# Kernel optimization log

Hardware: AMD Instinct MI355X
Metric: run time of the kernel (lower is better)

Reference implementation:

```python
import jax, jax.numpy as jnp
import numpy as np

B, N, C, HEADS = 8, 1024, 768, 12
HW = 32  # H = W = 32, so H*W == N


def _layernorm(x, g, b, eps=1e-5):
    mu = x.mean(-1, keepdims=True)
    var = ((x - mu) ** 2).mean(-1, keepdims=True)
    return (x - mu) * jax.lax.rsqrt(var + eps) * g + b


def setup_inputs() -> dict:
    key = jax.random.key(0)
    ks = jax.random.split(key, 6)
    w = lambda k, shape: jax.random.normal(k, shape, dtype=jnp.float32) * 0.02
    return {
        "x": jax.random.normal(ks[0], (B, N, C), dtype=jnp.float32),
        "y": jax.random.normal(ks[1], (B, C, HW, HW), dtype=jnp.float32),
        "q_w": w(ks[2], (C, C)),
        "q_b": jnp.zeros((C,), jnp.float32),
        "kv_w": w(ks[3], (2 * C, C)),
        "kv_b": jnp.zeros((2 * C,), jnp.float32),
        "proj_w": w(ks[4], (C, C)),
        "proj_b": jnp.zeros((C,), jnp.float32),
        "ln_g": jnp.ones((C,), jnp.float32),
        "ln_b": jnp.zeros((C,), jnp.float32),
        "H": HW,
        "W": HW,
    }


def reference(x, y, q_w, q_b, kv_w, kv_b, proj_w, proj_b, ln_g, ln_b, H, W):
    Bn, Nn, Cn = x.shape
    hd = Cn // HEADS
    scale = hd ** -0.5  # qk_scale=None, c_ratio=1 -> head_dim**-0.5

    # gating tensors from y
    y1 = y.reshape(Bn, Cn, H * W).transpose(0, 2, 1)          # [B, N, C]
    y2 = _layernorm(y1, ln_g, ln_b)
    yq = jax.nn.sigmoid(y2 @ q_w.T + q_b)                      # [B, N, C]
    ykv = jax.nn.sigmoid(y2 @ kv_w.T + kv_b)                   # [B, N, 2C]

    # gated q: q2 = q0 + q0*yq
    q0 = x @ q_w.T + q_b
    q = (q0 + q0 * yq).reshape(Bn, Nn, HEADS, hd).transpose(0, 2, 1, 3)  # [B,h,N,d]

    # gated kv: kv2 = kv0*ykv + ykv
    kv0 = x @ kv_w.T + kv_b
    kv = (kv0 * ykv + ykv).reshape(Bn, Nn, 2, HEADS, hd).transpose(2, 0, 3, 1, 4)
    k, v = kv[0], kv[1]                                        # [B,h,N,d] each

    attn = jax.nn.softmax(jnp.einsum("bhqd,bhkd->bhqk", q, k) * scale, axis=-1)
    out = jnp.einsum("bhqk,bhkd->bhqd", attn, v)
    out = out.transpose(0, 2, 1, 3).reshape(Bn, Nn, Cn)
    return out @ proj_w.T + proj_b
```

## Files before the change

### kernel.cpp

```cpp
#include <hip/hip_runtime.h>
#include <stdint.h>

typedef __attribute__((ext_vector_type(4))) float f4;
typedef __attribute__((ext_vector_type(8))) short bf16x8;
typedef __attribute__((ext_vector_type(4))) unsigned short u16x4;
typedef unsigned short u16;

#define B_ 8
#define N_ 1024
#define C_ 768
#define NH 12
#define HD 64

__device__ __forceinline__ float bf2f(u16 v) {
  union { unsigned u; float f; } x; x.u = ((unsigned)v) << 16; return x.f;
}
__device__ __forceinline__ u16 f2bf(float f) {
  union { float f; unsigned u; } x; x.f = f;
  unsigned r = x.u + 0x7FFFu + ((x.u >> 16) & 1u);
  return (u16)(r >> 16);
}
__device__ __forceinline__ void g2l16(const u16* g, const u16* l) {
  __builtin_amdgcn_global_load_lds(
      (const __attribute__((address_space(1))) void*)(uintptr_t)g,
      (__attribute__((address_space(3))) void*)(uint32_t)(uintptr_t)l,
      16, 0, 0);
}

#define SW12() asm volatile("s_waitcnt vmcnt(12)" ::: "memory")
#define SW6()  asm volatile("s_waitcnt vmcnt(6)" ::: "memory")
#define SW4()  asm volatile("s_waitcnt vmcnt(4)" ::: "memory")
#define SW3()  asm volatile("s_waitcnt vmcnt(3)" ::: "memory")
#define SW0()  asm volatile("s_waitcnt vmcnt(0)" ::: "memory")
#define BARF()                              \
  do {                                      \
    __builtin_amdgcn_s_barrier();           \
    asm volatile("" ::: "memory");          \
    __builtin_amdgcn_sched_barrier(0);      \
  } while (0)

__global__ __launch_bounds__(256) void cvt_bf16(const float* __restrict__ s,
                                                u16* __restrict__ d, int n4) {
  int i = blockIdx.x * 256 + threadIdx.x;
  int stride = gridDim.x * 256;
  for (; i < n4; i += stride) {
    float4 v = ((const float4*)s)[i];
    u16x4 o;
    o.x = f2bf(v.x); o.y = f2bf(v.y); o.z = f2bf(v.z); o.w = f2bf(v.w);
    ((u16x4*)d)[i] = o;
  }
}

__global__ __launch_bounds__(256) void ln_stats(const float* __restrict__ y,
                                                float* __restrict__ mu,
                                                float* __restrict__ rs,
                                                int b0) {
  __shared__ float s1[4][64], s2[4][64];
  int t = threadIdx.x;
  int nl = t & 63, ch = t >> 6;
  int idx0 = b0 * N_ + blockIdx.x * 64;
  int b = idx0 >> 10, nb_ = idx0 & 1023;
  const float* p = y + (size_t)b * C_ * N_ + nb_ + nl;
  float s = 0.f, q = 0.f;
  int c0 = ch * 192;
  for (int c = c0; c < c0 + 192; ++c) {
    float v = p[(size_t)c * N_];
    s += v; q += v * v;
  }
  s1[ch][nl] = s; s2[ch][nl] = q;
  __syncthreads();
  if (t < 64) {
    float ts = s1[0][t] + s1[1][t] + s1[2][t] + s1[3][t];
    float tq = s2[0][t] + s2[1][t] + s2[2][t] + s2[3][t];
    float m = ts * (1.f / C_);
    float var = tq * (1.f / C_) - m * m;
    mu[idx0 + t] = m;
    rs[idx0 + t] = rsqrtf(fmaxf(var, 0.f) + 1e-5f);
  }
}

__global__ __launch_bounds__(256) void ln_apply(const float* __restrict__ y,
                                                const float* __restrict__ mu,
                                                const float* __restrict__ rs,
                                                const float* __restrict__ lg,
                                                const float* __restrict__ lb,
                                                u16* __restrict__ y2c,
                                                int b0) {
  __shared__ float tile[64][65];
  int t = threadIdx.x;
  int n0 = blockIdx.x * 64, c0 = blockIdx.y * 64;
  int bl = blockIdx.z, b = b0 + bl;
  int jc = (t & 15) * 4, ir = t >> 4;
  for (int r = 0; r < 4; ++r) {
    int i = ir + r * 16;
    float4 v = *(const float4*)(y + ((size_t)b * C_ + c0 + i) * N_ + n0 + jc);
    tile[i][jc] = v.x; tile[i][jc + 1] = v.y; tile[i][jc + 2] = v.z; tile[i][jc + 3] = v.w;
  }
  __syncthreads();
  for (int r = 0; r < 4; ++r) {
    int i = ir + r * 16;
    int n = n0 + i;
    float m = mu[b * N_ + n], rr = rs[b * N_ + n];
    float g0 = lg[c0 + jc],     b0f = lb[c0 + jc];
    float g1 = lg[c0 + jc + 1], b1f = lb[c0 + jc + 1];
    float g2 = lg[c0 + jc + 2], b2f = lb[c0 + jc + 2];
    float g3 = lg[c0 + jc + 3], b3f = lb[c0 + jc + 3];
    u16x4 o;
    o.x = f2bf((tile[jc][i] - m) * rr * g0 + b0f);
    o.y = f2bf((tile[jc + 1][i] - m) * rr * g1 + b1f);
    o.z = f2bf((tile[jc + 2][i] - m) * rr * g2 + b2f);
    o.w = f2bf((tile[jc + 3][i] - m) * rr * g3 + b3f);
    *(u16x4*)(y2c + ((size_t)bl * N_ + n) * C_ + c0 + jc) = o;
  }
}

__global__ __launch_bounds__(256, 2) void gemm_gate(
    const u16* __restrict__ xbc, const u16* __restrict__ y2c,
    const u16* __restrict__ qwb, const u16* __restrict__ kvwb,
    const float* __restrict__ qb_, const float* __restrict__ kvb_,
    u16* __restrict__ o_q, u16* __restrict__ o_k, u16* __restrict__ o_vT) {
  __shared__ u16 smem[36864];
  int t = threadIdx.x, l = t & 63;
  int quad = l >> 4, l15 = l & 15;
  int w = t >> 6, wm = w & 1, wn = w >> 1;
  int m0l = blockIdx.x * 128;
  int n0l = blockIdx.y * 128;

  const u16* wp; const float* bp; int sel, h0;
  if (n0l < C_) {
    wp = qwb + (size_t)n0l * C_; bp = qb_ + n0l; sel = 0; h0 = n0l >> 6;
  } else {
    int nk = n0l - C_;
    wp = kvwb + (size_t)nk * C_; bp = kvb_ + nk;
    sel = (nk < C_) ? 1 : 2;
    h0 = ((sel == 2) ? nk - C_ : nk) >> 6;
  }

  f4 accx[4][4], accy[4][4];
  for (int i = 0; i < 4; ++i)
    for (int j = 0; j < 4; ++j) {
      accx[i][j] = (f4){0.f, 0.f, 0.f, 0.f};
      accy[i][j] = (f4){0.f, 0.f, 0.f, 0.f};
    }

  int row = t >> 2;
  int colS = (((t & 3) ^ (row & 3)) * 8);
  const u16* gx = xbc + (size_t)(m0l + row) * C_ + colS;
  const u16* gy = y2c + (size_t)(m0l + row) * C_ + colS;
  const u16* gw = wp + (size_t)row * C_ + colS;
  int rsl = (quad ^ (l15 & 3)) * 8;

#define STAGE_G(OFF, kk)                                   \
  do {                                                     \
    u16* p_ = smem + (OFF);                                \
    g2l16(gx + (kk),           p_ + t * 8);                \
    g2l16(gx + (kk) + 64 * C_, p_ + 2048 + t * 8);         \
    g2l16(gy + (kk),           p_ + 4096 + t * 8);         \
    g2l16(gy + (kk) + 64 * C_, p_ + 6144 + t * 8);         \
    g2l16(gw + (kk),           p_ + 8192 + t * 8);         \
    g2l16(gw + (kk) + 64 * C_, p_ + 10240 + t * 8);        \
  } while (0)

#define COMPUTE_G(OFF)                                                        \
  do {                                                                        \
    const u16* base = smem + (OFF);                                           \
    bf16x8 afx[4], afy[4], bfr[4];                                            \
    for (int i = 0; i < 4; ++i) {                                             \
      int ra = (wm * 64 + i * 16 + l15) * 32 + rsl;                           \
      afx[i] = *(const bf16x8*)&base[ra];                                     \
      afy[i] = *(const bf16x8*)&base[4096 + ra];                              \
      int rb = (wn * 64 + i * 16 + l15) * 32 + rsl;                           \
      bfr[i] = *(const bf16x8*)&base[8192 + rb];                              \
    }                                                                         \
    for (int i = 0; i < 4; ++i)                                               \
      for (int j = 0; j < 4; ++j) {                                           \
        accx[i][j] = __builtin_amdgcn_mfma_f32_16x16x32_bf16(afx[i], bfr[j], accx[i][j], 0, 0, 0); \
        accy[i][j] = __builtin_amdgcn_mfma_f32_16x16x32_bf16(afy[i], bfr[j], accy[i][j], 0, 0, 0); \
      }                                                                       \
  } while (0)

#define STEP_G(i, OFF)                                        \
  do {                                                        \
    COMPUTE_G(OFF);                                           \
    BARF();                                                   \
    if ((i) < 21)      { STAGE_G(OFF, ((i) + 3) * 32); SW12(); } \
    else if ((i) == 21) SW6();                                \
    else if ((i) == 22) SW0();                                \
    BARF();                                                   \
  } while (0)

  STAGE_G(0, 0);
  STAGE_G(12288, 32);
  STAGE_G(24576, 64);
  SW12();
  BARF();
#pragma unroll
  for (int n = 0; n < 24; n += 3) {
    STEP_G(n, 0);
    STEP_G(n + 1, 12288);
    STEP_G(n + 2, 24576);
  }
#undef STEP_G
#undef STAGE_G
#undef COMPUTE_G

  const int PITCH = 136;
  for (int j = 0; j < 4; ++j) {
    int cloc = wn * 64 + j * 16 + l15;
    float bias = bp[cloc];
    for (int i = 0; i < 4; ++i) {
      int rb0 = wm * 64 + i * 16 + quad * 4;
      for (int r = 0; r < 4; ++r) {
        int rloc = rb0 + r;
        float vx = accx[i][j][r] + bias;
        float vy = accy[i][j][r] + bias;
        float gg = 1.f / (1.f + __expf(-vy));
        float val = (sel == 0) ? vx * (1.f + gg) : gg * (vx + 1.f);
        u16 bv = f2bf(val);
        if (sel == 2) smem[cloc * PITCH + rloc] = bv;
        else          smem[rloc * PITCH + cloc] = bv;
      }
    }
  }
  __syncthreads();
  {
    int rr = t >> 1, hh = t & 1;
    const u16* src = smem + rr * PITCH + hh * 64;
    u16* dst;
    if (sel == 2) {
      int h = h0 + (rr >> 6), d = rr & 63;
      int bl = m0l >> 10, nbase = m0l & 1023;
      dst = o_vT + (size_t)((bl * NH + h) * HD + d) * N_ + nbase + hh * 64;
    } else {
      int gml = m0l + rr;
      int bl = gml >> 10, n = gml & 1023;
      int h = h0 + hh;
      dst = (sel == 0 ? o_q : o_k) + (size_t)((bl * NH + h) * N_ + n) * HD;
    }
    for (int c = 0; c < 8; ++c) {
      bf16x8 v = *(const bf16x8*)(src + c * 8);
      *(bf16x8*)(dst + c * 8) = v;
    }
  }
}

__global__ __launch_bounds__(256) void attn(const u16* __restrict__ qoc,
                                            const u16* __restrict__ koc,
                                            const u16* __restrict__ vTc,
                                            u16* __restrict__ aoc) {
  __shared__ u16 Qs[4096], Ks[8192], Vs[8192];
  __shared__ u16 Ps[64 * 72];
  int t = threadIdx.x, l = t & 63, w = t >> 6;
  int quad = l >> 4, l15 = l & 15;
  int bhl = blockIdx.y;
  int bl = bhl / NH, h = bhl % NH;
  int q0 = blockIdx.x * 64;
  int sr = t >> 3;
  int swo = ((t & 7) ^ (sr & 7)) * 8;
  const u16* qbp = qoc + ((size_t)bhl * N_ + q0) * HD;
  const u16* kb = koc + (size_t)bhl * N_ * HD;
  const u16* vb = vTc + (size_t)bhl * HD * N_;

#define STAGE_KV(OFF, key0)                                                   \
  do {                                                                        \
    g2l16(kb + (size_t)((key0) + sr) * HD + swo,      Ks + (OFF) + t * 8);    \
    g2l16(kb + (size_t)((key0) + 32 + sr) * HD + swo, Ks + (OFF) + 2048 + t * 8); \
    g2l16(vb + (size_t)sr * N_ + (key0) + swo,        Vs + (OFF) + t * 8);    \
    g2l16(vb + (size_t)(32 + sr) * N_ + (key0) + swo, Vs + (OFF) + 2048 + t * 8); \
  } while (0)

  g2l16(qbp + sr * HD + swo,        Qs + t * 8);
  g2l16(qbp + (32 + sr) * HD + swo, Qs + 2048 + t * 8);
  STAGE_KV(0, 0);
  STAGE_KV(4096, 64);
  SW4();
  BARF();

  int sA = (quad ^ (l15 & 7)) * 8;
  int sB = sA ^ 32;
  bf16x8 aq0 = *(const bf16x8*)&Qs[(w * 16 + l15) * 64 + sA];
  bf16x8 aq1 = *(const bf16x8*)&Qs[(w * 16 + l15) * 64 + sB];
  f4 o[4];
  for (int i = 0; i < 4; ++i) o[i] = (f4){0.f, 0.f, 0.f, 0.f};
  f4 ls = (f4){0.f, 0.f, 0.f, 0.f};
  bf16x8 ones;
  for (int i = 0; i < 8; ++i) ones[i] = (short)0x3F80;

#define TILE_STEP(KOFF)                                                       \
  do {                                                                        \
    f4 s_[4];                                                                 \
    __builtin_amdgcn_s_setprio(1);                                            \
    for (int ni = 0; ni < 4; ++ni) {                                          \
      bf16x8 b0v = *(const bf16x8*)&Ks[(KOFF) + (ni * 16 + l15) * 64 + sA];   \
      bf16x8 b1v = *(const bf16x8*)&Ks[(KOFF) + (ni * 16 + l15) * 64 + sB];   \
      f4 z = (f4){0.f, 0.f, 0.f, 0.f};                                        \
      z = __builtin_amdgcn_mfma_f32_16x16x32_bf16(aq0, b0v, z, 0, 0, 0);      \
      z = __builtin_amdgcn_mfma_f32_16x16x32_bf16(aq1, b1v, z, 0, 0, 0);      \
      s_[ni] = z;                                                             \
    }                                                                         \
    __builtin_amdgcn_s_setprio(0);                                            \
    for (int ni = 0; ni < 4; ++ni)                                            \
      for (int r = 0; r < 4; ++r)                                             \
        Ps[(w * 16 + quad * 4 + r) * 72 + ni * 16 + l15] =                    \
            f2bf(__expf(s_[ni][r] * 0.125f));                                 \
    bf16x8 ap0 = *(const bf16x8*)&Ps[(w * 16 + l15) * 72 + quad * 8];         \
    bf16x8 ap1 = *(const bf16x8*)&Ps[(w * 16 + l15) * 72 + 32 + quad * 8];    \
    __builtin_amdgcn_s_setprio(1);                                            \
    for (int ni = 0; ni < 4; ++ni) {                                          \
      bf16x8 b0v = *(const bf16x8*)&Vs[(KOFF) + (ni * 16 + l15) * 64 + sA];   \
      bf16x8 b1v = *(const bf16x8*)&Vs[(KOFF) + (ni * 16 + l15) * 64 + sB];   \
      o[ni] = __builtin_amdgcn_mfma_f32_16x16x32_bf16(ap0, b0v, o[ni], 0, 0, 0); \
      o[ni] = __builtin_amdgcn_mfma_f32_16x16x32_bf16(ap1, b1v, o[ni], 0, 0, 0); \
    }                                                                         \
    ls = __builtin_amdgcn_mfma_f32_16x16x32_bf16(ap0, ones, ls, 0, 0, 0);     \
    ls = __builtin_amdgcn_mfma_f32_16x16x32_bf16(ap1, ones, ls, 0, 0, 0);     \
    __builtin_amdgcn_s_setprio(0);                                            \
  } while (0)

#pragma unroll
  for (int kt = 0; kt < 16; kt += 2) {
    TILE_STEP(0);
    BARF();
    if (kt + 2 < 16) { STAGE_KV(0, (kt + 2) * 64); SW4(); } else { SW0(); }
    BARF();
    TILE_STEP(4096);
    BARF();
    if (kt + 3 < 16) { STAGE_KV(4096, (kt + 3) * 64); SW4(); } else { SW0(); }
    BARF();
  }
#undef TILE_STEP
#undef STAGE_KV

  for (int ni = 0; ni < 4; ++ni)
    for (int r = 0; r < 4; ++r)
      Ps[(w * 16 + quad * 4 + r) * 72 + ni * 16 + l15] =
          f2bf(o[ni][r] / ls[r]);
  __syncthreads();
  {
    int rr = t >> 2, cc = t & 3;
    int n = q0 + rr;
    const u16* src = Ps + rr * 72 + cc * 16;
    u16* dst = aoc + ((size_t)bl * N_ + n) * C_ + h * HD + cc * 16;
    *(bf16x8*)dst = *(const bf16x8*)src;
    *(bf16x8*)(dst + 8) = *(const bf16x8*)(src + 8);
  }
}

__global__ __launch_bounds__(256, 2) void gemm_proj(const u16* __restrict__ aoc,
                                                    const u16* __restrict__ pwb,
                                                    const float* __restrict__ bias,
                                                    float* __restrict__ out,
                                                    int b0) {
  __shared__ u16 smem[18432];
  int t = threadIdx.x, l = t & 63;
  int quad = l >> 4, l15 = l & 15;
  int w = t >> 6, wm = w & 1, wn = w >> 1;
  int m0l = blockIdx.x * 128, n0 = blockIdx.y * 64;
  f4 acc[4][2];
  for (int i = 0; i < 4; ++i)
    for (int j = 0; j < 2; ++j) acc[i][j] = (f4){0.f, 0.f, 0.f, 0.f};
  int row = t >> 2;
  int colS = (((t & 3) ^ (row & 3)) * 8);
  const u16* ga = aoc + (size_t)(m0l + row) * C_ + colS;
  const u16* gw = pwb + (size_t)(n0 + row) * C_ + colS;
  int rsl = (quad ^ (l15 & 3)) * 8;

#define STAGE_P(OFF, kk)                                   \
  do {                                                     \
    u16* p_ = smem + (OFF);                                \
    g2l16(ga + (kk),           p_ + t * 8);                \
    g2l16(ga + (kk) + 64 * C_, p_ + 2048 + t * 8);         \
    g2l16(gw + (kk),           p_ + 4096 + t * 8);         \
  } while (0)

#define COMPUTE_P(OFF)                                                        \
  do {                                                                        \
    const u16* base = smem + (OFF);                                           \
    bf16x8 af[4], bfr[2];                                                     \
    for (int i = 0; i < 4; ++i)                                               \
      af[i] = *(const bf16x8*)&base[(wm * 64 + i * 16 + l15) * 32 + rsl];     \
    for (int j = 0; j < 2; ++j)                                               \
      bfr[j] = *(const bf16x8*)&base[4096 + (wn * 32 + j * 16 + l15) * 32 + rsl]; \
    for (int i = 0; i < 4; ++i)                                               \
      for (int j = 0; j < 2; ++j)                                             \
        acc[i][j] = __builtin_amdgcn_mfma_f32_16x16x32_bf16(af[i], bfr[j], acc[i][j], 0, 0, 0); \
  } while (0)

#define STEP_P(i, OFF)                                        \
  do {                                                        \
    COMPUTE_P(OFF);                                           \
    BARF();                                                   \
    if ((i) < 21)      { STAGE_P(OFF, ((i) + 3) * 32); SW6(); } \
    else if ((i) == 21) SW3();                                \
    else if ((i) == 22) SW0();                                \
    BARF();                                                   \
  } while (0)

  STAGE_P(0, 0);
  STAGE_P(6144, 32);
  STAGE_P(12288, 64);
  SW6();
  BARF();
#pragma unroll
  for (int n = 0; n < 24; n += 3) {
    STEP_P(n, 0);
    STEP_P(n + 1, 6144);
    STEP_P(n + 2, 12288);
  }
#undef STEP_P
#undef STAGE_P
#undef COMPUTE_P

  for (int j = 0; j < 2; ++j) {
    int gcol = n0 + wn * 32 + j * 16 + l15;
    float bv = bias[gcol];
    for (int i = 0; i < 4; ++i) {
      int rbase = m0l + wm * 64 + i * 16 + quad * 4;
      for (int r = 0; r < 4; ++r)
        __builtin_nontemporal_store(acc[i][j][r] + bv,
                                    &out[(size_t)(b0 * N_ + rbase + r) * C_ + gcol]);
    }
  }
}

extern "C" void kernel_launch(void* const* d_in, const int* in_sizes, int n_in,
                              void* d_out, int out_size, void* d_ws, size_t ws_size,
                              hipStream_t stream) {
  const float* x   = (const float*)d_in[0];
  const float* y   = (const float*)d_in[1];
  const float* qw  = (const float*)d_in[2];
  const float* qb  = (const float*)d_in[3];
  const float* kvw = (const float*)d_in[4];
  const float* kvb = (const float*)d_in[5];
  const float* pw  = (const float*)d_in[6];
  const float* pb  = (const float*)d_in[7];
  const float* lg  = (const float*)d_in[8];
  const float* lb  = (const float*)d_in[9];

  char* ws = (char*)d_ws;
  float* mu = (float*)(ws);
  float* rs = (float*)(ws + 32768);
  u16* qwb  = (u16*)(ws + 65536);
  u16* kvwb = (u16*)(ws + 1245184);
  u16* pwb  = (u16*)(ws + 3604480);
  const size_t BASE2 = 4784128;
  const size_t PER_B = 1572864;

  int nb = 1;
  for (int c = 8; c >= 1; c >>= 1) {
    if (BASE2 + 5 * (size_t)c * PER_B <= ws_size) { nb = c; break; }
  }
  u16* xbc = (u16*)(ws + BASE2);
  u16* y2c = (u16*)(ws + BASE2 + (size_t)nb * PER_B);
  u16* qoc = (u16*)(ws + BASE2 + 2 * (size_t)nb * PER_B);
  u16* koc = (u16*)(ws + BASE2 + 3 * (size_t)nb * PER_B);
  u16* vTc = (u16*)(ws + BASE2 + 4 * (size_t)nb * PER_B);
  u16* aoc = xbc;

  cvt_bf16<<<dim3(576), dim3(256), 0, stream>>>(qw, qwb, 147456);
  cvt_bf16<<<dim3(1152), dim3(256), 0, stream>>>(kvw, kvwb, 294912);
  cvt_bf16<<<dim3(576), dim3(256), 0, stream>>>(pw, pwb, 147456);

  for (int b0 = 0; b0 < B_; b0 += nb) {
    cvt_bf16<<<dim3(768 * nb), dim3(256), 0, stream>>>(
        x + (size_t)b0 * N_ * C_, xbc, nb * 196608);
    ln_stats<<<dim3(16 * nb), dim3(256), 0, stream>>>(y, mu, rs, b0);
    ln_apply<<<dim3(16, 12, nb), dim3(256), 0, stream>>>(y, mu, rs, lg, lb, y2c, b0);
    gemm_gate<<<dim3(8 * nb, 18), dim3(256), 0, stream>>>(xbc, y2c, qwb, kvwb,
                                                          qb, kvb, qoc, koc, vTc);
    attn<<<dim3(16, 12 * nb), dim3(256), 0, stream>>>(qoc, koc, vTc, aoc);
    gemm_proj<<<dim3(8 * nb, 12), dim3(256), 0, stream>>>(aoc, pwb, pb, (float*)d_out, b0);
  }
}
```

Before: 285.3 us.

## Fuse layernorm stats and apply; simplify proj pipeline to double-buffer

Replaces the two-pass layernorm (stats kernel plus transpose/apply kernel) with one kernel that reads each y column once, keeps a bf16 copy in LDS, computes mean/rstd, then writes the normalized transposed output. This removes a second read of y and one launch. It also removes the unroll pragma on the attention loop, and cuts the projection GEMM from triple to double buffering without the LDS swizzle. That lowers LDS use but may add bank conflicts and reduce load/compute overlap. Rounding y to bf16 before normalization adds a little error.

```diff
diff --git a/kernel.cpp b/kernel.cpp
--- a/kernel.cpp
+++ b/kernel.cpp
@@ -51,66 +51,50 @@
   }
 }
 
-__global__ __launch_bounds__(256) void ln_stats(const float* __restrict__ y,
-                                                float* __restrict__ mu,
-                                                float* __restrict__ rs,
-                                                int b0) {
-  __shared__ float s1[4][64], s2[4][64];
-  int t = threadIdx.x;
-  int nl = t & 63, ch = t >> 6;
-  int idx0 = b0 * N_ + blockIdx.x * 64;
-  int b = idx0 >> 10, nb_ = idx0 & 1023;
-  const float* p = y + (size_t)b * C_ * N_ + nb_ + nl;
-  float s = 0.f, q = 0.f;
-  int c0 = ch * 192;
-  for (int c = c0; c < c0 + 192; ++c) {
-    float v = p[(size_t)c * N_];
-    s += v; q += v * v;
-  }
-  s1[ch][nl] = s; s2[ch][nl] = q;
-  __syncthreads();
-  if (t < 64) {
-    float ts = s1[0][t] + s1[1][t] + s1[2][t] + s1[3][t];
-    float tq = s2[0][t] + s2[1][t] + s2[2][t] + s2[3][t];
-    float m = ts * (1.f / C_);
-    float var = tq * (1.f / C_) - m * m;
-    mu[idx0 + t] = m;
-    rs[idx0 + t] = rsqrtf(fmaxf(var, 0.f) + 1e-5f);
-  }
-}
-
-__global__ __launch_bounds__(256) void ln_apply(const float* __restrict__ y,
-                                                const float* __restrict__ mu,
-                                                const float* __restrict__ rs,
+__global__ __launch_bounds__(512) void ln_fused(const float* __restrict__ y,
                                                 const float* __restrict__ lg,
                                                 const float* __restrict__ lb,
                                                 u16* __restrict__ y2c,
                                                 int b0) {
-  __shared__ float tile[64][65];
+  __shared__ u16 ybuf[768 * 33];
+  __shared__ float ps[16][32], pq[16][32];
+  __shared__ float smu[32], srs[32];
   int t = threadIdx.x;
-  int n0 = blockIdx.x * 64, c0 = blockIdx.y * 64;
-  int bl = blockIdx.z, b = b0 + bl;
-  int jc = (t & 15) * 4, ir = t >> 4;
-  for (int r = 0; r < 4; ++r) {
-    int i = ir + r * 16;
-    float4 v = *(const float4*)(y + ((size_t)b * C_ + c0 + i) * N_ + n0 + jc);
-    tile[i][jc] = v.x; tile[i][jc + 1] = v.y; tile[i][jc + 2] = v.z; tile[i][jc + 3] = v.w;
-  }
+  int nl = t & 31, ch = t >> 5;
+  int idx0 = b0 * N_ + blockIdx.x * 32;
+  int b = idx0 >> 10, nb_ = idx0 & 1023;
+  const float* p = y + (size_t)b * C_ * N_ + nb_ + nl;
+  float s = 0.f, q = 0.f;
+  int c0 = ch * 48;
+  for (int c = c0; c < c0 + 48; ++c) {
+    float v = p[(size_t)c * N_];
+    s += v; q += v * v;
+    ybuf[c * 33 + nl] = f2bf(v);
+  }
+  ps[ch][nl] = s; pq[ch][nl] = q;
   __syncthreads();
-  for (int r = 0; r < 4; ++r) {
-    int i = ir + r * 16;
-    int n = n0 + i;
-    float m = mu[b * N_ + n], rr = rs[b * N_ + n];
-    float g0 = lg[c0 + jc],     b0f = lb[c0 + jc];
-    float g1 = lg[c0 + jc + 1], b1f = lb[c0 + jc + 1];
-    float g2 = lg[c0 + jc + 2], b2f = lb[c0 + jc + 2];
-    float g3 = lg[c0 + jc + 3], b3f = lb[c0 + jc + 3];
-    u16x4 o;
-    o.x = f2bf((tile[jc][i] - m) * rr * g0 + b0f);
-    o.y = f2bf((tile[jc + 1][i] - m) * rr * g1 + b1f);
-    o.z = f2bf((tile[jc + 2][i] - m) * rr * g2 + b2f);
-    o.w = f2bf((tile[jc + 3][i] - m) * rr * g3 + b3f);
-    *(u16x4*)(y2c + ((size_t)bl * N_ + n) * C_ + c0 + jc) = o;
+  if (t < 32) {
+    float ts = 0.f, tq = 0.f;
+    for (int g = 0; g < 16; ++g) { ts += ps[g][t]; tq += pq[g][t]; }
+    float m = ts * (1.f / C_);
+    float var = tq * (1.f / C_) - m * m;
+    smu[t] = m;
+    srs[t] = rsqrtf(fmaxf(var, 0.f) + 1e-5f);
+  }
+  __syncthreads();
+  int rn = t >> 4, cg = t & 15;
+  float m = smu[rn], rr = srs[rn];
+  int bl = b - b0;
+  int n = nb_ + rn;
+  u16* dst = y2c + ((size_t)bl * N_ + n) * C_ + cg * 48;
+  for (int cc = 0; cc < 48; cc += 8) {
+    int c = cg * 48 + cc;
+    bf16x8 o;
+    for (int j = 0; j < 8; ++j) {
+      float v = bf2f(ybuf[(c + j) * 33 + rn]);
+      o[j] = (short)f2bf((v - m) * rr * lg[c + j] + lb[c + j]);
+    }
+    *(bf16x8*)(dst + cc) = o;
   }
 }
 
@@ -317,7 +301,6 @@
     __builtin_amdgcn_s_setprio(0);                                            \
   } while (0)
 
-#pragma unroll
   for (int kt = 0; kt < 16; kt += 2) {
     TILE_STEP(0);
     BARF();
@@ -351,7 +334,7 @@
                                                     const float* __restrict__ bias,
                                                     float* __restrict__ out,
                                                     int b0) {
-  __shared__ u16 smem[18432];
+  __shared__ u16 smem[12288];
   int t = threadIdx.x, l = t & 63;
   int quad = l >> 4, l15 = l & 15;
   int w = t >> 6, wm = w & 1, wn = w >> 1;
@@ -359,11 +342,9 @@
   f4 acc[4][2];
   for (int i = 0; i < 4; ++i)
     for (int j = 0; j < 2; ++j) acc[i][j] = (f4){0.f, 0.f, 0.f, 0.f};
-  int row = t >> 2;
-  int colS = (((t & 3) ^ (row & 3)) * 8);
-  const u16* ga = aoc + (size_t)(m0l + row) * C_ + colS;
-  const u16* gw = pwb + (size_t)(n0 + row) * C_ + colS;
-  int rsl = (quad ^ (l15 & 3)) * 8;
+  int row = t >> 2, colb = (t & 3) * 8;
+  const u16* ga = aoc + (size_t)(m0l + row) * C_ + colb;
+  const u16* gw = pwb + (size_t)(n0 + row) * C_ + colb;
 
 #define STAGE_P(OFF, kk)                                   \
   do {                                                     \
@@ -378,36 +359,28 @@
     const u16* base = smem + (OFF);                                           \
     bf16x8 af[4], bfr[2];                                                     \
     for (int i = 0; i < 4; ++i)                                               \
-      af[i] = *(const bf16x8*)&base[(wm * 64 + i * 16 + l15) * 32 + rsl];     \
+      af[i] = *(const bf16x8*)&base[(wm * 64 + i * 16 + l15) * 32 + quad * 8];\
     for (int j = 0; j < 2; ++j)                                               \
-      bfr[j] = *(const bf16x8*)&base[4096 + (wn * 32 + j * 16 + l15) * 32 + rsl]; \
+      bfr[j] = *(const bf16x8*)&base[4096 + (wn * 32 + j * 16 + l15) * 32 + quad * 8]; \
     for (int i = 0; i < 4; ++i)                                               \
       for (int j = 0; j < 2; ++j)                                             \
         acc[i][j] = __builtin_amdgcn_mfma_f32_16x16x32_bf16(af[i], bfr[j], acc[i][j], 0, 0, 0); \
   } while (0)
 
-#define STEP_P(i, OFF)                                        \
-  do {                                                        \
-    COMPUTE_P(OFF);                                           \
-    BARF();                                                   \
-    if ((i) < 21)      { STAGE_P(OFF, ((i) + 3) * 32); SW6(); } \
-    else if ((i) == 21) SW3();                                \
-    else if ((i) == 22) SW0();                                \
-    BARF();                                                   \
-  } while (0)
-
   STAGE_P(0, 0);
   STAGE_P(6144, 32);
-  STAGE_P(12288, 64);
-  SW6();
+  SW3();
   BARF();
-#pragma unroll
-  for (int n = 0; n < 24; n += 3) {
-    STEP_P(n, 0);
-    STEP_P(n + 1, 6144);
-    STEP_P(n + 2, 12288);
-  }
-#undef STEP_P
+  for (int n = 0; n < 24; n += 2) {
+    COMPUTE_P(0);
+    BARF();
+    if (n + 2 < 24) { STAGE_P(0, (n + 2) * 32); SW3(); } else { SW0(); }
+    BARF();
+    COMPUTE_P(6144);
+    BARF();
+    if (n + 3 < 24) { STAGE_P(6144, (n + 3) * 32); SW3(); } else { SW0(); }
+    BARF();
+  }
 #undef STAGE_P
 #undef COMPUTE_P
 
@@ -438,8 +411,6 @@
   const float* lb  = (const float*)d_in[9];
 
   char* ws = (char*)d_ws;
-  float* mu = (float*)(ws);
-  float* rs = (float*)(ws + 32768);
   u16* qwb  = (u16*)(ws + 65536);
   u16* kvwb = (u16*)(ws + 1245184);
   u16* pwb  = (u16*)(ws + 3604480);
@@ -464,8 +435,7 @@
   for (int b0 = 0; b0 < B_; b0 += nb) {
     cvt_bf16<<<dim3(768 * nb), dim3(256), 0, stream>>>(
         x + (size_t)b0 * N_ * C_, xbc, nb * 196608);
-    ln_stats<<<dim3(16 * nb), dim3(256), 0, stream>>>(y, mu, rs, b0);
-    ln_apply<<<dim3(16, 12, nb), dim3(256), 0, stream>>>(y, mu, rs, lg, lb, y2c, b0);
+    ln_fused<<<dim3(32 * nb), dim3(512), 0, stream>>>(y, lg, lb, y2c, b0);
     gemm_gate<<<dim3(8 * nb, 18), dim3(256), 0, stream>>>(xbc, y2c, qwb, kvwb,
                                                           qb, kvb, qoc, koc, vTc);
     attn<<<dim3(16, 12 * nb), dim3(256), 0, stream>>>(qoc, koc, vTc, aoc);
```

Result: faster. 276.1 us (-3.2%).
